# Performance work log

Measured on AMD Instinct MI355X. Metric: run time of the kernel, lower is better.

Reference implementation:

```python
import jax, jax.numpy as jnp
import numpy as np

N_NODES = 50000
N_EDGES = 800000
D = 128        # input_dim == output_dim
D_EDGE = 64    # edge_attr_size
Z_DIM = 2 * D + D_EDGE  # 320


def setup_inputs() -> dict:
    key = jax.random.key(0)
    k1, k2, k3, k4, k5 = jax.random.split(key, 5)
    x = jax.random.normal(k1, (N_NODES, D), dtype=jnp.float32)
    edge_index = jax.random.randint(k2, (2, N_EDGES), 0, N_NODES, dtype=jnp.int64)
    edge_attr = jax.random.normal(k3, (N_EDGES, D_EDGE), dtype=jnp.float32)
    scale = 1.0 / np.sqrt(Z_DIM)
    W_f = jax.random.normal(k4, (Z_DIM, D), dtype=jnp.float32) * scale
    W_s = jax.random.normal(k5, (Z_DIM, D), dtype=jnp.float32) * scale
    b_f = jnp.zeros((D,), dtype=jnp.float32)
    b_s = jnp.zeros((D,), dtype=jnp.float32)
    return {"x": x, "edge_index": edge_index, "edge_attr": edge_attr,
            "W_f": W_f, "b_f": b_f, "W_s": W_s, "b_s": b_s}


def reference(x, edge_index, edge_attr, W_f, b_f, W_s, b_s):
    # Dropout(p=0.0) is identity in inference.
    src = edge_index[0]  # j (message source)
    dst = edge_index[1]  # i (message target)
    # z_e = [x_i, x_j, e_ij]  -> [E, 2D + D_edge]
    z = jnp.concatenate([x[dst], x[src], edge_attr], axis=-1)
    # CGConv message: sigmoid(lin_f(z)) * softplus(lin_s(z))
    msg = jax.nn.sigmoid(z @ W_f + b_f) * jax.nn.softplus(z @ W_s + b_s)
    # scatter-add aggregation + residual
    out = jax.ops.segment_sum(msg, dst, num_segments=x.shape[0]) + x
    # use_activation=True -> ReLU
    return jax.nn.relu(out)
```

## Files before the change

### kernel.cpp

```cpp
#include <hip/hip_runtime.h>
#include <hip/hip_bf16.h>

#define E_TOTAL   800000
#define NN        50000
#define DD        128
#define DE        64
#define ZDIM      320
#define KE        192
#define MT        64
#define NBS       196

typedef short bf16x8 __attribute__((ext_vector_type(8)));
typedef float f32x4  __attribute__((ext_vector_type(4)));

__device__ __forceinline__ unsigned short f2bf(float f) {
    union { float f; unsigned int u; } v; v.f = f;
    unsigned int u = v.u;
    return (unsigned short)((u + 0x7fffu + ((u >> 16) & 1u)) >> 16);
}

__device__ __forceinline__ float bf2f(unsigned short h) {
    union { unsigned u; float f; } v; v.u = ((unsigned)h) << 16; return v.f;
}

__device__ __forceinline__ unsigned pkbf2(float a, float b) {
    __hip_bfloat162 h = __float22bfloat162_rn(make_float2(a, b));
    unsigned u; __builtin_memcpy(&u, &h, 4); return u;
}

__device__ __forceinline__ uint2 pkbf4(float4 v) {
    uint2 r; r.x = pkbf2(v.x, v.y); r.y = pkbf2(v.z, v.w); return r;
}

__device__ __forceinline__ float fast_rcp(float x) {
#if __has_builtin(__builtin_amdgcn_rcpf)
    return __builtin_amdgcn_rcpf(x);
#else
    return 1.0f / x;
#endif
}


__global__ void scan_part(const int* __restrict__ counts, int* __restrict__ partial) {
    __shared__ int red[256];
    int t = threadIdx.x, k = blockIdx.x * 256 + t;
    red[t] = (k < NN) ? counts[k] : 0;
    __syncthreads();
    for (int d = 128; d > 0; d >>= 1) {
        if (t < d) red[t] += red[t + d];
        __syncthreads();
    }
    if (t == 0) partial[blockIdx.x] = red[0];
}

__global__ void scan_top(int* __restrict__ partial) {
    __shared__ int s[256];
    int t = threadIdx.x;
    int v = (t < NBS) ? partial[t] : 0;
    s[t] = v; __syncthreads();
    for (int d = 1; d < 256; d <<= 1) {
        int a = (t >= d) ? s[t - d] : 0;
        __syncthreads();
        s[t] += a;
        __syncthreads();
    }
    if (t < NBS) partial[t] = s[t] - v;
}

__global__ void scan_final(const int* __restrict__ counts,
                           const int* __restrict__ partial,
                           int* __restrict__ cursor) {
    __shared__ int s[256];
    int t = threadIdx.x, k = blockIdx.x * 256 + t;
    int v = (k < NN) ? counts[k] : 0;
    s[t] = v; __syncthreads();
    for (int d = 1; d < 256; d <<= 1) {
        int a = (t >= d) ? s[t - d] : 0;
        __syncthreads();
        s[t] += a;
        __syncthreads();
    }
    if (k < NN) cursor[k] = partial[blockIdx.x] + s[t] - v;
}

__global__ void scatter_kernel(const int* __restrict__ ei, int* __restrict__ cursor,
                               uint2* __restrict__ spak2) {
    int e = blockIdx.x * 256 + threadIdx.x;
    if (e < E_TOTAL) {
        int d = ei[E_TOTAL + e];
        int pos = atomicAdd(&cursor[d], 1);
        uint2 p; p.x = ((unsigned)d << 16) | (unsigned)ei[e]; p.y = (unsigned)e;
        spak2[pos] = p;
    }
}


__global__ void prep_kernel2(const float* __restrict__ x,
                             const int* __restrict__ ei,
                             const float* __restrict__ W_f,
                             const float* __restrict__ W_s,
                             unsigned short* __restrict__ WtE,
                             unsigned short* __restrict__ WtN,
                             int* __restrict__ counts,
                             float* __restrict__ out) {
    int id = blockIdx.x * 256 + threadIdx.x;
    ((float4*)out)[id] = ((const float4*)x)[id];
    if (id < E_TOTAL) atomicAdd(&counts[ei[E_TOTAL + id]], 1);
    if (id < 256 * DE) {
        int n = id >> 6, k = id & 63;
        int ok = 2 * DD + k;
        float wv = (n < DD) ? W_f[ok * DD + n] : W_s[ok * DD + (n - DD)];
        WtE[id] = f2bf(wv);
    } else if (id < 256 * DE + 2 * 256 * DD) {
        int id2 = id - 256 * DE;
        int part = id2 >> 15;
        int r = id2 & 32767;
        int n = r >> 7, k = r & 127;
        int ok = part * DD + k;
        float wv = (n < DD) ? W_f[ok * DD + n] : W_s[ok * DD + (n - DD)];
        WtN[id2] = f2bf(wv);
    }
}

__global__ __launch_bounds__(256, 4)
void node_kernel2(const float* __restrict__ x,
                  const unsigned short* __restrict__ WtN,
                  const float* __restrict__ bf_, const float* __restrict__ bs_,
                  unsigned int* __restrict__ nodeP32) {
    __shared__ unsigned short A_lds[MT * DD];
    const int t = threadIdx.x;
    const int m_off = blockIdx.x * MT;
    const int part = blockIdx.y;
    const int lane = t & 63, w = t >> 6, l15 = lane & 15, quad = lane >> 4;

    #pragma unroll
    for (int it = 0; it < 8; ++it) {
        int idx = it * 256 + t;
        int e = idx >> 5, kq = idx & 31;
        int row = m_off + e; if (row >= NN) row = NN - 1;
        float4 v = ((const float4*)(x + (size_t)row * DD))[kq];
        int g = kq >> 1;
        int col = ((g & ~7) | ((g & 7) ^ (e & 7))) * 8 + (kq & 1) * 4;
        *((uint2*)&A_lds[e * DD + col]) = pkbf4(v);
    }

    f32x4 acc[4][4] = {};
    const int nt0 = 2 * w;
    const unsigned short* Bp[4];
    #pragma unroll
    for (int u = 0; u < 4; ++u) {
        int nt = nt0 + ((u < 2) ? u : (6 + u));
        Bp[u] = WtN + (size_t)part * (256 * DD) +
                (size_t)(nt * 16 + l15) * DD + quad * 8;
    }
    __syncthreads();

    #pragma unroll
    for (int ks = 0; ks < 4; ++ks) {
        bf16x8 af[4], bfr[4];
        #pragma unroll
        for (int i = 0; i < 4; ++i) {
            int m = i * 16 + l15;
            int g = 4 * ks + quad;
            int col = ((g & ~7) | ((g & 7) ^ (l15 & 7))) * 8;
            af[i] = *((const bf16x8*)&A_lds[m * DD + col]);
        }
        #pragma unroll
        for (int u = 0; u < 4; ++u)
            bfr[u] = *((const bf16x8*)(Bp[u] + ks * 32));
        #pragma unroll
        for (int i = 0; i < 4; ++i)
            #pragma unroll
            for (int u = 0; u < 4; ++u)
                acc[i][u] = __builtin_amdgcn_mfma_f32_16x16x32_bf16(
                    af[i], bfr[u], acc[i][u], 0, 0, 0);
    }

    const int c0 = 32 * w + l15, c1 = c0 + 16;
    const float bf0 = part ? 0.f : bf_[c0], bs0 = part ? 0.f : bs_[c0];
    const float bf1 = part ? 0.f : bf_[c1], bs1 = part ? 0.f : bs_[c1];
    #pragma unroll
    for (int i = 0; i < 4; ++i)
        #pragma unroll
        for (int j = 0; j < 4; ++j) {
            int e = i * 16 + quad * 4 + j;
            int row = m_off + e;
            if (row < NN) {
                unsigned int* np = nodeP32 + (size_t)row * 256 + part * 128;
                np[c0] = pkbf2(acc[i][0][j] + bf0, acc[i][2][j] + bs0);
                np[c1] = pkbf2(acc[i][1][j] + bf1, acc[i][3][j] + bs1);
            }
        }
}

__global__ __launch_bounds__(512, 4)
void edge_kernel2(const float* __restrict__ ea,
                  const unsigned short* __restrict__ WtE,
                  const unsigned int* __restrict__ nodeP32,
                  float* __restrict__ out,
                  const uint2* __restrict__ spak2) {
    __shared__ float sumb[MT][DD];
    __shared__ unsigned short A_lds[MT * DE];
    __shared__ int dst_lds[MT];
    __shared__ int src_lds[MT];
    __shared__ int eid_lds[MT];
    __shared__ int runid_lds[MT];
    __shared__ int rdst_lds[MT];
    __shared__ int rbound_lds[MT];
    __shared__ int ndist_lds;

    const int t = threadIdx.x;
    const int m_off = blockIdx.x * MT;
    const int lane = t & 63, w2 = t >> 6, l15 = lane & 15, quad = lane >> 4;

    if (t < MT) {
        uint2 p = spak2[m_off + t];
        int dsv = (int)(p.x >> 16);
        dst_lds[t] = dsv;
        src_lds[t] = (int)(p.x & 0xffffu);
        eid_lds[t] = (int)p.y;
        int updsv = __shfl_up(dsv, 1);
        int flag = (t == 0 || dsv != updsv) ? 1 : 0;
        unsigned long long m = __ballot(flag != 0);
        int rid = __popcll(m << (63 - t)) - 1;
        runid_lds[t] = rid;
        if (flag) { rdst_lds[rid] = dsv; rbound_lds[rid] = 0; }
        int nd = __popcll(m);
        if (t == 0) {
            ndist_lds = nd;
            if (m_off > 0 &&
                (int)(spak2[m_off - 1].x >> 16) == dsv)
                rbound_lds[0] = 1;
        }
        if (t == MT - 1) {
            if (m_off + MT < E_TOTAL &&
                (int)(spak2[m_off + MT].x >> 16) == dsv)
                rbound_lds[nd - 1] = 1;
        }
    }
    __syncthreads();

    const int c = 16 * w2 + l15;

    float4 va[2];
    #pragma unroll
    for (int it = 0; it < 2; ++it) {
        int idx = it * 512 + t;
        int e = idx >> 4;
        va[it] = ((const float4*)(ea + (size_t)eid_lds[e] * DE))[idx & 15];
    }
    unsigned int ps[16], pd[16];
    #pragma unroll
    for (int i = 0; i < 4; ++i)
        #pragma unroll
        for (int j = 0; j < 4; ++j) {
            int e = i * 16 + quad * 4 + j;
            ps[i * 4 + j] = nodeP32[(size_t)src_lds[e] * 256 + 128 + c];
            pd[i * 4 + j] = nodeP32[(size_t)dst_lds[e] * 256 + c];
        }
    {
        int nd = ndist_lds;
        int col = t & 127, rb = t >> 7;
        for (int r = rb; r < nd; r += 4) sumb[r][col] = 0.f;
    }
    #pragma unroll
    for (int it = 0; it < 2; ++it) {
        int idx = it * 512 + t;
        int e = idx >> 4, kq = idx & 15;
        int g = kq >> 1;
        int col = ((g & 7) ^ (e & 7)) * 8 + (kq & 1) * 4;
        *((uint2*)&A_lds[e * DE + col]) = pkbf4(va[it]);
    }

    f32x4 acc[4][2] = {};
    const unsigned short* Bp[2];
    #pragma unroll
    for (int u = 0; u < 2; ++u) {
        int nt = w2 + u * 8;
        Bp[u] = WtE + (size_t)(nt * 16 + l15) * DE + quad * 8;
    }
    __syncthreads();

    #pragma unroll
    for (int ks = 0; ks < 2; ++ks) {
        bf16x8 af[4], bfr[2];
        #pragma unroll
        for (int i = 0; i < 4; ++i) {
            int m = i * 16 + l15;
            int g = 4 * ks + quad;
            int col = ((g & 7) ^ (l15 & 7)) * 8;
            af[i] = *((const bf16x8*)&A_lds[m * DE + col]);
        }
        #pragma unroll
        for (int u = 0; u < 2; ++u)
            bfr[u] = *((const bf16x8*)(Bp[u] + ks * 32));
        #pragma unroll
        for (int i = 0; i < 4; ++i)
            #pragma unroll
            for (int u = 0; u < 2; ++u)
                acc[i][u] = __builtin_amdgcn_mfma_f32_16x16x32_bf16(
                    af[i], bfr[u], acc[i][u], 0, 0, 0);
    }

    int rprev = -1;
    float s0 = 0.f, nf = 0.f, ns = 0.f;
    #pragma unroll
    for (int i = 0; i < 4; ++i)
        #pragma unroll
        for (int j = 0; j < 4; ++j) {
            int e = i * 16 + quad * 4 + j;
            int rid = runid_lds[e];
            if (rid != rprev) {
                if (rprev >= 0) atomicAdd(&sumb[rprev][c], s0);
                rprev = rid; s0 = 0.f;
                unsigned int pk = pd[i * 4 + j];
                nf = bf2f((unsigned short)(pk & 0xffffu));
                ns = bf2f((unsigned short)(pk >> 16));
            }
            unsigned int pp = ps[i * 4 + j];
            float f  = acc[i][0][j] + nf + bf2f((unsigned short)(pp & 0xffffu));
            float sg = acc[i][1][j] + ns + bf2f((unsigned short)(pp >> 16));
            s0 += fast_rcp(1.f + __expf(-f)) *
                  (fmaxf(sg, 0.f) + __logf(1.f + __expf(-fabsf(sg))));
        }
    atomicAdd(&sumb[rprev][c], s0);
    __syncthreads();

    {
        int nd = ndist_lds;
        int col = t & 127, rb = t >> 7;
        for (int r = rb; r < nd; r += 4) {
            float v = sumb[r][col];
            float* op = out + (size_t)rdst_lds[r] * DD + col;
            if (rbound_lds[r]) atomicAdd(op, v);
            else *op += v;
        }
    }
}


__global__ void prep_kernel(const float* __restrict__ x,
                            const int* __restrict__ ei,
                            const float* __restrict__ W_f,
                            const float* __restrict__ W_s,
                            unsigned short* __restrict__ WtE,
                            unsigned short* __restrict__ WtN,
                            int* __restrict__ counts,
                            float* __restrict__ out) {
    int id = blockIdx.x * 256 + threadIdx.x;
    ((float4*)out)[id] = ((const float4*)x)[id];
    if (id < E_TOTAL) atomicAdd(&counts[ei[E_TOTAL + id]], 1);
    if (id < 256 * KE) {
        int n = id / KE, k = id - n * KE;
        int ok = 128 + k;
        float wv = (n < DD) ? W_f[ok * DD + n] : W_s[ok * DD + (n - DD)];
        WtE[id] = f2bf(wv);
    } else if (id < 256 * KE + 256 * DD) {
        int id2 = id - 256 * KE;
        int n = id2 / DD, k = id2 - n * DD;
        float wv = (n < DD) ? W_f[k * DD + n] : W_s[k * DD + (n - DD)];
        WtN[id2] = f2bf(wv);
    }
}

__global__ __launch_bounds__(256, 4)
void node_kernel(const float* __restrict__ x,
                 const unsigned short* __restrict__ WtN,
                 const float* __restrict__ bf_, const float* __restrict__ bs_,
                 unsigned short* __restrict__ nodeP) {
    __shared__ unsigned short A_lds[MT * DD];
    const int t = threadIdx.x;
    const int m_off = blockIdx.x * MT;
    const int lane = t & 63, w = t >> 6, l15 = lane & 15, quad = lane >> 4;

    #pragma unroll
    for (int it = 0; it < 8; ++it) {
        int idx = it * 256 + t;
        int e = idx >> 5, kq = idx & 31;
        int row = m_off + e; if (row >= NN) row = NN - 1;
        float4 v = ((const float4*)(x + (size_t)row * DD))[kq];
        int g = kq >> 1;
        int col = ((g & ~7) | ((g & 7) ^ (e & 7))) * 8 + (kq & 1) * 4;
        *((uint2*)&A_lds[e * DD + col]) = pkbf4(v);
    }

    f32x4 acc[4][4] = {};
    const int nt0 = 2 * w;
    const unsigned short* Bp[4];
    #pragma unroll
    for (int u = 0; u < 4; ++u) {
        int nt = nt0 + ((u < 2) ? u : (6 + u));
        Bp[u] = WtN + (size_t)(nt * 16 + l15) * DD + quad * 8;
    }
    __syncthreads();

    #pragma unroll
    for (int ks = 0; ks < 4; ++ks) {
        bf16x8 af[4], bfr[4];
        #pragma unroll
        for (int i = 0; i < 4; ++i) {
            int m = i * 16 + l15;
            int g = 4 * ks + quad;
            int col = ((g & ~7) | ((g & 7) ^ (l15 & 7))) * 8;
            af[i] = *((const bf16x8*)&A_lds[m * DD + col]);
        }
        #pragma unroll
        for (int u = 0; u < 4; ++u)
            bfr[u] = *((const bf16x8*)(Bp[u] + ks * 32));
        #pragma unroll
        for (int i = 0; i < 4; ++i)
            #pragma unroll
            for (int u = 0; u < 4; ++u)
                acc[i][u] = __builtin_amdgcn_mfma_f32_16x16x32_bf16(
                    af[i], bfr[u], acc[i][u], 0, 0, 0);
    }

    const int c0 = 32 * w + l15, c1 = c0 + 16;
    const float bf0 = bf_[c0], bs0 = bs_[c0], bf1 = bf_[c1], bs1 = bs_[c1];
    #pragma unroll
    for (int i = 0; i < 4; ++i)
        #pragma unroll
        for (int j = 0; j < 4; ++j) {
            int e = i * 16 + quad * 4 + j;
            int row = m_off + e;
            if (row < NN) {
                uint2 pk;
                pk.x = pkbf2(acc[i][0][j] + bf0, acc[i][1][j] + bf1);
                pk.y = pkbf2(acc[i][2][j] + bs0, acc[i][3][j] + bs1);
                *((uint2*)(nodeP + (size_t)row * 256 + w * 64 + l15 * 4)) = pk;
            }
        }
}

__global__ __launch_bounds__(256, 4)
void edge_kernel(const float* __restrict__ x,
                 const float* __restrict__ ea,
                 const unsigned short* __restrict__ WtE,
                 const unsigned short* __restrict__ nodeP,
                 float* __restrict__ out,
                 const uint2* __restrict__ spak2) {
    __shared__ unsigned short A_lds[MT * KE];
    __shared__ int dst_lds[MT];
    __shared__ int src_lds[MT];
    __shared__ int eid_lds[MT];

    const int t = threadIdx.x;
    const int m_off = blockIdx.x * MT;
    const int lane = t & 63, w = t >> 6, l15 = lane & 15, quad = lane >> 4;

    if (t < MT) {
        uint2 p = spak2[m_off + t];
        dst_lds[t] = (int)(p.x >> 16);
        src_lds[t] = (int)(p.x & 0xffffu);
        eid_lds[t] = (int)p.y;
    }
    __syncthreads();

    #pragma unroll
    for (int it = 0; it < 4; ++it) {
        int idx = it * 256 + t;
        int e = idx >> 4, kq = idx & 15;
        float4 v = ((const float4*)(ea + (size_t)eid_lds[e] * DE))[kq];
        int g = 16 + (kq >> 1);
        int col = ((g & ~7) | ((g & 7) ^ (e & 7))) * 8 + (kq & 1) * 4;
        *((uint2*)&A_lds[e * KE + col]) = pkbf4(v);
    }
    #pragma unroll
    for (int it = 0; it < 8; ++it) {
        int idx = it * 256 + t;
        int e = idx >> 5, kq = idx & 31;
        float4 v = ((const float4*)(x + (size_t)src_lds[e] * DD))[kq];
        int g = kq >> 1;
        int col = ((g & ~7) | ((g & 7) ^ (e & 7))) * 8 + (kq & 1) * 4;
        *((uint2*)&A_lds[e * KE + col]) = pkbf4(v);
    }

    f32x4 acc[4][4] = {};
    const int nt0 = 2 * w;
    const unsigned short* Bp[4];
    #pragma unroll
    for (int u = 0; u < 4; ++u) {
        int nt = nt0 + ((u < 2) ? u : (6 + u));
        Bp[u] = WtE + (size_t)(nt * 16 + l15) * KE + quad * 8;
    }
    __syncthreads();

    #pragma unroll
    for (int ks = 0; ks < 6; ++ks) {
        bf16x8 af[4], bfr[4];
        #pragma unroll
        for (int i = 0; i < 4; ++i) {
            int m = i * 16 + l15;
            int g = 4 * ks + quad;
            int col = ((g & ~7) | ((g & 7) ^ (l15 & 7))) * 8;
            af[i] = *((const bf16x8*)&A_lds[m * KE + col]);
        }
        #pragma unroll
        for (int u = 0; u < 4; ++u)
            bfr[u] = *((const bf16x8*)(Bp[u] + ks * 32));
        #pragma unroll
        for (int i = 0; i < 4; ++i)
            #pragma unroll
            for (int u = 0; u < 4; ++u)
                acc[i][u] = __builtin_amdgcn_mfma_f32_16x16x32_bf16(
                    af[i], bfr[u], acc[i][u], 0, 0, 0);
    }

    const int c0 = 32 * w + l15, c1 = c0 + 16;
    const int np_off = w * 64 + l15 * 4;

    int d = -1;
    float s0 = 0.f, s1 = 0.f, nf0 = 0.f, ns0 = 0.f, nf1 = 0.f, ns1 = 0.f;
    #pragma unroll
    for (int i = 0; i < 4; ++i)
        #pragma unroll
        for (int j = 0; j < 4; ++j) {
            int e = i * 16 + quad * 4 + j;
            int dd = dst_lds[e];
            if (dd != d) {
                if (d >= 0) {
                    atomicAdd(out + (size_t)d * DD + c0, s0);
                    atomicAdd(out + (size_t)d * DD + c1, s1);
                }
                d = dd; s0 = 0.f; s1 = 0.f;
                uint2 pk = *((const uint2*)(nodeP + (size_t)d * 256 + np_off));
                nf0 = bf2f((unsigned short)(pk.x & 0xffffu));
                nf1 = bf2f((unsigned short)(pk.x >> 16));
                ns0 = bf2f((unsigned short)(pk.y & 0xffffu));
                ns1 = bf2f((unsigned short)(pk.y >> 16));
            }
            float f0  = acc[i][0][j] + nf0;
            float sg0 = acc[i][2][j] + ns0;
            s0 += fast_rcp(1.f + __expf(-f0)) *
                  (fmaxf(sg0, 0.f) + __logf(1.f + __expf(-fabsf(sg0))));
            float f1  = acc[i][1][j] + nf1;
            float sg1 = acc[i][3][j] + ns1;
            s1 += fast_rcp(1.f + __expf(-f1)) *
                  (fmaxf(sg1, 0.f) + __logf(1.f + __expf(-fabsf(sg1))));
        }
    atomicAdd(out + (size_t)d * DD + c0, s0);
    atomicAdd(out + (size_t)d * DD + c1, s1);
}

__global__ void relu_kernel(float* __restrict__ out) {
    int id = blockIdx.x * 256 + threadIdx.x;
    if (id < NN * DD / 4) {
        float4 v = ((float4*)out)[id];
        v.x = fmaxf(v.x, 0.0f); v.y = fmaxf(v.y, 0.0f);
        v.z = fmaxf(v.z, 0.0f); v.w = fmaxf(v.w, 0.0f);
        ((float4*)out)[id] = v;
    }
}


__global__ void prep_fb(const float* __restrict__ x,
                        const float* __restrict__ W_f,
                        const float* __restrict__ W_s,
                        unsigned short* __restrict__ Wt,
                        float* __restrict__ out) {
    int id = blockIdx.x * 256 + threadIdx.x;
    if (id < NN * DD / 4)
        ((float4*)out)[id] = ((const float4*)x)[id];
    if (id < 2 * DD * ZDIM) {
        int n = id / ZDIM, k = id - n * ZDIM;
        float wv = (n < DD) ? W_f[k * DD + n] : W_s[k * DD + (n - DD)];
        Wt[n * ZDIM + k] = f2bf(wv);
    }
}

__global__ __launch_bounds__(256, 3)
void edge_fb(const float* __restrict__ x,
             const int* __restrict__ ei,
             const float* __restrict__ ea,
             const unsigned short* __restrict__ Wt,
             const float* __restrict__ bf_,
             const float* __restrict__ bs_,
             float* __restrict__ out) {
    __shared__ unsigned short A_lds[MT * ZDIM];
    __shared__ int dst_lds[MT];
    __shared__ int src_lds[MT];

    const int t = threadIdx.x;
    const int m_off = blockIdx.x * MT;
    const int lane = t & 63, w = t >> 6, l15 = lane & 15, quad = lane >> 4;

    if (t < MT) dst_lds[t] = ei[E_TOTAL + m_off + t];
    else if (t < 2 * MT) src_lds[t - MT] = ei[m_off + (t - MT)];
    __syncthreads();

    #pragma unroll
    for (int it = 0; it < 4; ++it) {
        int idx = it * 256 + t;
        int e = idx >> 4, kq = idx & 15;
        float4 v = ((const float4*)(ea + (size_t)(m_off + e) * DE))[kq];
        int g = 32 + (kq >> 1);
        int col = ((g & ~7) | ((g & 7) ^ (e & 7))) * 8 + (kq & 1) * 4;
        *((uint2*)&A_lds[e * ZDIM + col]) = pkbf4(v);
    }
    #pragma unroll
    for (int it = 0; it < 8; ++it) {
        int idx = it * 256 + t;
        int e = idx >> 5, kq = idx & 31;
        float4 v = ((const float4*)(x + (size_t)dst_lds[e] * DD))[kq];
        int g = kq >> 1;
        int col = ((g & ~7) | ((g & 7) ^ (e & 7))) * 8 + (kq & 1) * 4;
        *((uint2*)&A_lds[e * ZDIM + col]) = pkbf4(v);
    }
    #pragma unroll
    for (int it = 0; it < 8; ++it) {
        int idx = it * 256 + t;
        int e = idx >> 5, kq = idx & 31;
        float4 v = ((const float4*)(x + (size_t)src_lds[e] * DD))[kq];
        int g = 16 + (kq >> 1);
        int col = ((g & ~7) | ((g & 7) ^ (e & 7))) * 8 + (kq & 1) * 4;
        *((uint2*)&A_lds[e * ZDIM + col]) = pkbf4(v);
    }

    f32x4 acc[4][4] = {};
    const int nt0 = 2 * w;
    const unsigned short* Bp[4];
    #pragma unroll
    for (int u = 0; u < 4; ++u) {
        int nt = nt0 + ((u < 2) ? u : (6 + u));
        Bp[u] = Wt + (size_t)(nt * 16 + l15) * ZDIM + quad * 8;
    }
    __syncthreads();

    #pragma unroll
    for (int ks = 0; ks < 10; ++ks) {
        bf16x8 af[4], bfr[4];
        #pragma unroll
        for (int i = 0; i < 4; ++i) {
            int m = i * 16 + l15;
            int g = 4 * ks + quad;
            int col = ((g & ~7) | ((g & 7) ^ (l15 & 7))) * 8;
            af[i] = *((const bf16x8*)&A_lds[m * ZDIM + col]);
        }
        #pragma unroll
        for (int u = 0; u < 4; ++u)
            bfr[u] = *((const bf16x8*)(Bp[u] + ks * 32));
        #pragma unroll
        for (int i = 0; i < 4; ++i)
            #pragma unroll
            for (int u = 0; u < 4; ++u)
                acc[i][u] = __builtin_amdgcn_mfma_f32_16x16x32_bf16(
                    af[i], bfr[u], acc[i][u], 0, 0, 0);
    }

    const int c0 = 32 * w + l15, c1 = c0 + 16;
    const float bf0 = bf_[c0], bs0 = bs_[c0], bf1 = bf_[c1], bs1 = bs_[c1];
    #pragma unroll
    for (int i = 0; i < 4; ++i)
        #pragma unroll
        for (int j = 0; j < 4; ++j) {
            int e = i * 16 + quad * 4 + j;
            float* op = out + (size_t)dst_lds[e] * DD;
            float f0 = acc[i][0][j] + bf0;
            float sg0 = acc[i][2][j] + bs0;
            atomicAdd(op + c0, fast_rcp(1.f + __expf(-f0)) *
                (fmaxf(sg0, 0.f) + __logf(1.f + __expf(-fabsf(sg0)))));
            float f1 = acc[i][1][j] + bf1;
            float sg1 = acc[i][3][j] + bs1;
            atomicAdd(op + c1, fast_rcp(1.f + __expf(-f1)) *
                (fmaxf(sg1, 0.f) + __logf(1.f + __expf(-fabsf(sg1)))));
        }
}


extern "C" void kernel_launch(void* const* d_in, const int* in_sizes, int n_in,
                              void* d_out, int out_size, void* d_ws, size_t ws_size,
                              hipStream_t stream) {
    (void)in_sizes; (void)n_in; (void)out_size;
    const float* x   = (const float*)d_in[0];
    const int*   ei  = (const int*)d_in[1];
    const float* ea  = (const float*)d_in[2];
    const float* W_f = (const float*)d_in[3];
    const float* b_f = (const float*)d_in[4];
    const float* W_s = (const float*)d_in[5];
    const float* b_s = (const float*)d_in[6];
    float* out = (float*)d_out;

    char* ws = (char*)d_ws;
    const size_t WS_NEED2 = 58164864;
    const size_t WS_NEED1 = 32564864;

    if (ws_size >= WS_NEED2) {
        unsigned short* WtE2   = (unsigned short*)ws;
        unsigned short* WtN2   = (unsigned short*)(ws + 32768);
        int*            counts = (int*)(ws + 163840);
        int*            cursor = (int*)(ws + 363840);
        int*            partial= (int*)(ws + 563840);
        uint2*          spak2  = (uint2*)(ws + 564864);
        unsigned int*   nodeP32= (unsigned int*)(ws + 6964864);

        hipMemsetAsync(counts, 0, NN * sizeof(int), stream);
        prep_kernel2<<<NN * DD / 4 / 256, 256, 0, stream>>>(
            x, ei, W_f, W_s, WtE2, WtN2, counts, out);
        scan_part<<<NBS, 256, 0, stream>>>(counts, partial);
        scan_top<<<1, 256, 0, stream>>>(partial);
        scan_final<<<NBS, 256, 0, stream>>>(counts, partial, cursor);
        scatter_kernel<<<(E_TOTAL + 255) / 256, 256, 0, stream>>>(ei, cursor, spak2);
        dim3 ng((NN + MT - 1) / MT, 2);
        node_kernel2<<<ng, 256, 0, stream>>>(x, WtN2, b_f, b_s, nodeP32);
        edge_kernel2<<<E_TOTAL / MT, 512, 0, stream>>>(
            ea, WtE2, nodeP32, out, spak2);
    } else if (ws_size >= WS_NEED1) {
        unsigned short* WtE    = (unsigned short*)ws;
        unsigned short* WtN    = (unsigned short*)(ws + 98304);
        int*            counts = (int*)(ws + 163840);
        int*            cursor = (int*)(ws + 363840);
        int*            partial= (int*)(ws + 563840);
        uint2*          spak2  = (uint2*)(ws + 564864);
        unsigned short* nodeP  = (unsigned short*)(ws + 6964864);

        hipMemsetAsync(counts, 0, NN * sizeof(int), stream);
        prep_kernel<<<NN * DD / 4 / 256, 256, 0, stream>>>(
            x, ei, W_f, W_s, WtE, WtN, counts, out);
        scan_part<<<NBS, 256, 0, stream>>>(counts, partial);
        scan_top<<<1, 256, 0, stream>>>(partial);
        scan_final<<<NBS, 256, 0, stream>>>(counts, partial, cursor);
        scatter_kernel<<<(E_TOTAL + 255) / 256, 256, 0, stream>>>(ei, cursor, spak2);
        node_kernel<<<(NN + MT - 1) / MT, 256, 0, stream>>>(x, WtN, b_f, b_s, nodeP);
        edge_kernel<<<E_TOTAL / MT, 256, 0, stream>>>(
            x, ea, WtE, nodeP, out, spak2);
    } else {
        unsigned short* Wt = (unsigned short*)ws;
        prep_fb<<<6250, 256, 0, stream>>>(x, W_f, W_s, Wt, out);
        edge_fb<<<E_TOTAL / MT, 256, 0, stream>>>(x, ei, ea, Wt, b_f, b_s, out);
    }

    relu_kernel<<<6250, 256, 0, stream>>>(out);
}
```

Baseline: 606.7 us.

## Pre-permute edge attributes to bf16 in scatter pass, merge scan kernels, widen node kernel

The scatter pass now also converts edge_attr to bf16 and writes it, already swizzled, into the destination-sorted order. The edge kernel can then load its A tile with one contiguous 16-byte load per thread instead of gathering fp32 rows by edge id. The scan_top and scan_final kernels are merged into one, and the node kernel computes both weight halves in a single 512-thread block. This adds a 100MB workspace requirement and an extra bf16 write pass over edge attributes, in exchange for halving and linearizing the edge kernel's attribute reads.

Result: slower. 637.7 us (+5.1%).

```diff
diff --git a/kernel.cpp b/kernel.cpp
--- a/kernel.cpp
+++ b/kernel.cpp
@@ -38,6 +38,13 @@
 #else
     return 1.0f / x;
 #endif
+}
+
+__device__ __forceinline__ void barrier_lgkm() {
+    __builtin_amdgcn_sched_barrier(0);
+    asm volatile("s_waitcnt lgkmcnt(0)" ::: "memory");
+    __builtin_amdgcn_s_barrier();
+    __builtin_amdgcn_sched_barrier(0);
 }
 
 
@@ -83,6 +90,31 @@
     if (k < NN) cursor[k] = partial[blockIdx.x] + s[t] - v;
 }
 
+__global__ void scan_final2(const int* __restrict__ counts,
+                            const int* __restrict__ partial,
+                            int* __restrict__ cursor) {
+    __shared__ int s[256], p2[256], orig[256];
+    int t = threadIdx.x, k = blockIdx.x * 256 + t;
+    int pv = (t < NBS) ? partial[t] : 0;
+    p2[t] = pv; orig[t] = pv; __syncthreads();
+    for (int d = 1; d < 256; d <<= 1) {
+        int a = (t >= d) ? p2[t - d] : 0;
+        __syncthreads();
+        p2[t] += a;
+        __syncthreads();
+    }
+    int blkoff = p2[blockIdx.x] - orig[blockIdx.x];
+    int v = (k < NN) ? counts[k] : 0;
+    s[t] = v; __syncthreads();
+    for (int d = 1; d < 256; d <<= 1) {
+        int a = (t >= d) ? s[t - d] : 0;
+        __syncthreads();
+        s[t] += a;
+        __syncthreads();
+    }
+    if (k < NN) cursor[k] = blkoff + s[t] - v;
+}
+
 __global__ void scatter_kernel(const int* __restrict__ ei, int* __restrict__ cursor,
                                uint2* __restrict__ spak2) {
     int e = blockIdx.x * 256 + threadIdx.x;
@@ -91,6 +123,36 @@
         int pos = atomicAdd(&cursor[d], 1);
         uint2 p; p.x = ((unsigned)d << 16) | (unsigned)ei[e]; p.y = (unsigned)e;
         spak2[pos] = p;
+    }
+}
+
+__global__ __launch_bounds__(256)
+void scatter_kernel3(const int* __restrict__ ei, int* __restrict__ cursor,
+                     uint2* __restrict__ spak2,
+                     const float* __restrict__ ea,
+                     unsigned short* __restrict__ eaP) {
+    __shared__ int pos_lds[MT];
+    const int t = threadIdx.x;
+    const int eb = blockIdx.x * MT;
+    if (t < MT) {
+        int e_g = eb + t;
+        int d = ei[E_TOTAL + e_g];
+        int pos = atomicAdd(&cursor[d], 1);
+        uint2 p; p.x = ((unsigned)d << 16) | (unsigned)ei[e_g]; p.y = (unsigned)e_g;
+        spak2[pos] = p;
+        pos_lds[t] = pos;
+    }
+    __syncthreads();
+    const float4* ea4 = (const float4*)ea;
+    #pragma unroll
+    for (int jj = 0; jj < 4; ++jj) {
+        int f4 = ((t >> 6) * 4 + jj) * 64 + (t & 63);
+        int el = f4 >> 4, kq = f4 & 15;
+        float4 v = ea4[(size_t)(eb + el) * 16 + kq];
+        int pos = pos_lds[el];
+        int erow = pos & 63;
+        int col = (((kq >> 1) & 7) ^ (erow & 7)) * 8 + (kq & 1) * 4;
+        *((uint2*)(eaP + (size_t)(pos >> 6) * 4096 + erow * 64 + col)) = pkbf4(v);
     }
 }
 
@@ -122,6 +184,78 @@
     }
 }
 
+__global__ __launch_bounds__(512, 4)
+void node_kernel3(const float* __restrict__ x,
+                  const unsigned short* __restrict__ WtN,
+                  const float* __restrict__ bf_, const float* __restrict__ bs_,
+                  unsigned int* __restrict__ nodeP32) {
+    __shared__ unsigned short A_lds[MT * DD];
+    const int t = threadIdx.x;
+    const int m_off = blockIdx.x * MT;
+    const int lane = t & 63, w8 = t >> 6;
+    const int part = w8 >> 2, w = w8 & 3;
+    const int l15 = lane & 15, quad = lane >> 4;
+
+    #pragma unroll
+    for (int it = 0; it < 4; ++it) {
+        int idx = it * 512 + t;
+        int e = idx >> 5, kq = idx & 31;
+        int row = m_off + e; if (row >= NN) row = NN - 1;
+        float4 v = ((const float4*)(x + (size_t)row * DD))[kq];
+        int g = kq >> 1;
+        int col = ((g & ~7) | ((g & 7) ^ (e & 7))) * 8 + (kq & 1) * 4;
+        *((uint2*)&A_lds[e * DD + col]) = pkbf4(v);
+    }
+
+    f32x4 acc[4][4] = {};
+    const int nt0 = 2 * w;
+    const unsigned short* Bp[4];
+    #pragma unroll
+    for (int u = 0; u < 4; ++u) {
+        int nt = nt0 + ((u < 2) ? u : (6 + u));
+        Bp[u] = WtN + (size_t)part * (256 * DD) +
+                (size_t)(nt * 16 + l15) * DD + quad * 8;
+    }
+    __syncthreads();
+
+    #pragma unroll
+    for (int ks = 0; ks < 4; ++ks) {
+        bf16x8 af[4], bfr[4];
+        #pragma unroll
+        for (int i = 0; i < 4; ++i) {
+            int m = i * 16 + l15;
+            int g = 4 * ks + quad;
+            int col = ((g & ~7) | ((g & 7) ^ (l15 & 7))) * 8;
+            af[i] = *((const bf16x8*)&A_lds[m * DD + col]);
+        }
+        #pragma unroll
+        for (int u = 0; u < 4; ++u)
+            bfr[u] = *((const bf16x8*)(Bp[u] + ks * 32));
+        #pragma unroll
+        for (int i = 0; i < 4; ++i)
+            #pragma unroll
+            for (int u = 0; u < 4; ++u)
+                acc[i][u] = __builtin_amdgcn_mfma_f32_16x16x32_bf16(
+                    af[i], bfr[u], acc[i][u], 0, 0, 0);
+    }
+
+    const int c0 = 32 * w + l15, c1 = c0 + 16;
+    const float bf0 = part ? 0.f : bf_[c0], bs0 = part ? 0.f : bs_[c0];
+    const float bf1 = part ? 0.f : bf_[c1], bs1 = part ? 0.f : bs_[c1];
+    #pragma unroll
+    for (int i = 0; i < 4; ++i)
+        #pragma unroll
+        for (int j = 0; j < 4; ++j) {
+            int e = i * 16 + quad * 4 + j;
+            int row = m_off + e;
+            if (row < NN) {
+                unsigned int* np = nodeP32 + (size_t)row * 256 + part * 128;
+                np[c0] = pkbf2(acc[i][0][j] + bf0, acc[i][2][j] + bs0);
+                np[c1] = pkbf2(acc[i][1][j] + bf1, acc[i][3][j] + bs1);
+            }
+        }
+}
+
 __global__ __launch_bounds__(256, 4)
 void node_kernel2(const float* __restrict__ x,
                   const unsigned short* __restrict__ WtN,
@@ -191,6 +325,136 @@
                 np[c1] = pkbf2(acc[i][1][j] + bf1, acc[i][3][j] + bs1);
             }
         }
+}
+
+__global__ __launch_bounds__(512, 4)
+void edge_kernel3(const unsigned short* __restrict__ eaP,
+                  const unsigned short* __restrict__ WtE,
+                  const unsigned int* __restrict__ nodeP32,
+                  float* __restrict__ out,
+                  const uint2* __restrict__ spak2) {
+    __shared__ float sumb[MT][DD];
+    __shared__ alignas(16) unsigned short A_lds[MT * DE];
+    __shared__ int dst_lds[MT];
+    __shared__ int src_lds[MT];
+    __shared__ int runid_lds[MT];
+    __shared__ int rdst_lds[MT];
+    __shared__ int rbound_lds[MT];
+    __shared__ int ndist_lds;
+
+    const int t = threadIdx.x;
+    const int m_off = blockIdx.x * MT;
+    const int lane = t & 63, w2 = t >> 6, l15 = lane & 15, quad = lane >> 4;
+
+    if (t < MT) {
+        uint2 p = spak2[m_off + t];
+        int dsv = (int)(p.x >> 16);
+        dst_lds[t] = dsv;
+        src_lds[t] = (int)(p.x & 0xffffu);
+        int updsv = __shfl_up(dsv, 1);
+        int flag = (t == 0 || dsv != updsv) ? 1 : 0;
+        unsigned long long m = __ballot(flag != 0);
+        int rid = __popcll(m << (63 - t)) - 1;
+        runid_lds[t] = rid;
+        if (flag) { rdst_lds[rid] = dsv; rbound_lds[rid] = 0; }
+        int nd = __popcll(m);
+        if (t == 0) {
+            ndist_lds = nd;
+            if (m_off > 0 && (int)(spak2[m_off - 1].x >> 16) == dsv)
+                rbound_lds[0] = 1;
+        }
+        if (t == MT - 1) {
+            if (m_off + MT < E_TOTAL &&
+                (int)(spak2[m_off + MT].x >> 16) == dsv)
+                rbound_lds[nd - 1] = 1;
+        }
+    }
+    barrier_lgkm();
+
+    const int c = 16 * w2 + l15;
+
+    uint4 av = ((const uint4*)eaP)[(size_t)blockIdx.x * 512 + t];
+    __builtin_amdgcn_sched_barrier(0);
+    unsigned int ps[16], pd[16];
+    #pragma unroll
+    for (int i = 0; i < 4; ++i)
+        #pragma unroll
+        for (int j = 0; j < 4; ++j) {
+            int e = i * 16 + quad * 4 + j;
+            ps[i * 4 + j] = nodeP32[(size_t)src_lds[e] * 256 + 128 + c];
+            pd[i * 4 + j] = nodeP32[(size_t)dst_lds[e] * 256 + c];
+        }
+    {
+        int nd = ndist_lds;
+        int col = t & 127, rb = t >> 7;
+        for (int r = rb; r < nd; r += 4) sumb[r][col] = 0.f;
+    }
+    ((uint4*)A_lds)[t] = av;
+
+    f32x4 acc[4][2] = {};
+    const unsigned short* Bp[2];
+    #pragma unroll
+    for (int u = 0; u < 2; ++u) {
+        int nt = w2 + u * 8;
+        Bp[u] = WtE + (size_t)(nt * 16 + l15) * DE + quad * 8;
+    }
+    barrier_lgkm();
+
+    #pragma unroll
+    for (int ks = 0; ks < 2; ++ks) {
+        bf16x8 af[4], bfr[2];
+        #pragma unroll
+        for (int i = 0; i < 4; ++i) {
+            int m = i * 16 + l15;
+            int g = 4 * ks + quad;
+            int col = ((g & 7) ^ (l15 & 7)) * 8;
+            af[i] = *((const bf16x8*)&A_lds[m * DE + col]);
+        }
+        #pragma unroll
+        for (int u = 0; u < 2; ++u)
+            bfr[u] = *((const bf16x8*)(Bp[u] + ks * 32));
+        #pragma unroll
+        for (int i = 0; i < 4; ++i)
+            #pragma unroll
+            for (int u = 0; u < 2; ++u)
+                acc[i][u] = __builtin_amdgcn_mfma_f32_16x16x32_bf16(
+                    af[i], bfr[u], acc[i][u], 0, 0, 0);
+    }
+
+    int rprev = -1;
+    float s0 = 0.f, nf = 0.f, ns = 0.f;
+    #pragma unroll
+    for (int i = 0; i < 4; ++i)
+        #pragma unroll
+        for (int j = 0; j < 4; ++j) {
+            int e = i * 16 + quad * 4 + j;
+            int rid = runid_lds[e];
+            if (rid != rprev) {
+                if (rprev >= 0) atomicAdd(&sumb[rprev][c], s0);
+                rprev = rid; s0 = 0.f;
+                unsigned int pk = pd[i * 4 + j];
+                nf = bf2f((unsigned short)(pk & 0xffffu));
+                ns = bf2f((unsigned short)(pk >> 16));
+            }
+            unsigned int pp = ps[i * 4 + j];
+            float f  = acc[i][0][j] + nf + bf2f((unsigned short)(pp & 0xffffu));
+            float sg = acc[i][1][j] + ns + bf2f((unsigned short)(pp >> 16));
+            s0 += fast_rcp(1.f + __expf(-f)) *
+                  (fmaxf(sg, 0.f) + __logf(1.f + __expf(-fabsf(sg))));
+        }
+    atomicAdd(&sumb[rprev][c], s0);
+    barrier_lgkm();
+
+    {
+        int nd = ndist_lds;
+        int col = t & 127, rb = t >> 7;
+        for (int r = rb; r < nd; r += 4) {
+            float v = sumb[r][col];
+            float* op = out + (size_t)rdst_lds[r] * DD + col;
+            if (rbound_lds[r]) atomicAdd(op, v);
+            else *op += v;
+        }
+    }
 }
 
 __global__ __launch_bounds__(512, 4)
@@ -228,8 +492,7 @@
         int nd = __popcll(m);
         if (t == 0) {
             ndist_lds = nd;
-            if (m_off > 0 &&
-                (int)(spak2[m_off - 1].x >> 16) == dsv)
+            if (m_off > 0 && (int)(spak2[m_off - 1].x >> 16) == dsv)
                 rbound_lds[0] = 1;
         }
         if (t == MT - 1) {
@@ -681,10 +944,32 @@
     float* out = (float*)d_out;
 
     char* ws = (char*)d_ws;
+    const size_t WS_NEED3 = 160564864;
     const size_t WS_NEED2 = 58164864;
     const size_t WS_NEED1 = 32564864;
 
-    if (ws_size >= WS_NEED2) {
+    if (ws_size >= WS_NEED3) {
+        unsigned short* WtE2   = (unsigned short*)ws;
+        unsigned short* WtN2   = (unsigned short*)(ws + 32768);
+        int*            counts = (int*)(ws + 163840);
+        int*            cursor = (int*)(ws + 363840);
+        int*            partial= (int*)(ws + 563840);
+        uint2*          spak2  = (uint2*)(ws + 564864);
+        unsigned int*   nodeP32= (unsigned int*)(ws + 6964864);
+        unsigned short* eaP    = (unsigned short*)(ws + 58164864);
+
+        hipMemsetAsync(counts, 0, NN * sizeof(int), stream);
+        prep_kernel2<<<NN * DD / 4 / 256, 256, 0, stream>>>(
+            x, ei, W_f, W_s, WtE2, WtN2, counts, out);
+        scan_part<<<NBS, 256, 0, stream>>>(counts, partial);
+        scan_final2<<<NBS, 256, 0, stream>>>(counts, partial, cursor);
+        scatter_kernel3<<<E_TOTAL / MT, 256, 0, stream>>>(
+            ei, cursor, spak2, ea, eaP);
+        node_kernel3<<<(NN + MT - 1) / MT, 512, 0, stream>>>(
+            x, WtN2, b_f, b_s, nodeP32);
+        edge_kernel3<<<E_TOTAL / MT, 512, 0, stream>>>(
+            eaP, WtE2, nodeP32, out, spak2);
+    } else if (ws_size >= WS_NEED2) {
         unsigned short* WtE2   = (unsigned short*)ws;
         unsigned short* WtN2   = (unsigned short*)(ws + 32768);
         int*            counts = (int*)(ws + 163840);
```
